# Kernel optimization log

Hardware: AMD Instinct MI355X
Metric: run time of the kernel (lower is better)

## Reference

```python
import jax, jax.numpy as jnp
import numpy as np

N_NODES = 50000
N_EDGES = 800000
GNN_IN, GNN_HID, COMB = 256, 64, 64
MLP_IN, MLP_HID = 256, 512


def glorot(key, shape):
    fan_in, fan_out = shape[0], shape[1]
    s = jnp.sqrt(6.0 / (fan_in + fan_out)).astype(jnp.float32)
    return jax.random.uniform(key, shape, jnp.float32, -s, s)


def setup_inputs() -> dict:
    key = jax.random.key(0)
    ks = jax.random.split(key, 12)
    x = jax.random.normal(ks[0], (N_NODES, GNN_IN), jnp.float32)
    edge_index = jax.random.randint(ks[1], (2, N_EDGES), 0, N_NODES, jnp.int64 if jax.config.jax_enable_x64 else jnp.int32)
    edge_attr = jax.random.uniform(ks[2], (N_EDGES,), jnp.float32)
    user_features = jax.random.normal(ks[3], (N_NODES, MLP_IN), jnp.float32)
    params = {
        'gcn1_W': glorot(ks[4], (GNN_IN, GNN_HID)),
        'gcn1_b': jnp.zeros((GNN_HID,), jnp.float32),
        'gcn2_W': glorot(ks[5], (GNN_HID, COMB)),
        'gcn2_b': jnp.zeros((COMB,), jnp.float32),
        'fc1_W': glorot(ks[6], (MLP_IN, MLP_HID)),
        'fc1_b': jnp.zeros((MLP_HID,), jnp.float32),
        'fc2_W': glorot(ks[7], (MLP_HID, COMB)),
        'fc2_b': jnp.zeros((COMB,), jnp.float32),
        'fcf_W': glorot(ks[8], (2 * COMB, 1)),
        'fcf_b': jnp.zeros((1,), jnp.float32),
    }
    return dict(x=x, edge_index=edge_index, edge_attr=edge_attr,
                user_features=user_features, **params)


def gcn_conv(x, W, b, src, dst, ew, n_nodes):
    # PyG GCNConv: transform, add self-loops (weight 1), sym-normalize, scatter-add.
    h = x @ W  # [N, out]
    loop = jnp.arange(n_nodes, dtype=src.dtype)
    src_sl = jnp.concatenate([src, loop])
    dst_sl = jnp.concatenate([dst, loop])
    ew_sl = jnp.concatenate([ew, jnp.ones((n_nodes,), ew.dtype)])
    deg = jax.ops.segment_sum(ew_sl, dst_sl, num_segments=n_nodes)
    dinv = jnp.where(deg > 0, jax.lax.rsqrt(jnp.maximum(deg, 1e-12)), 0.0)
    norm = dinv[src_sl] * ew_sl * dinv[dst_sl]  # [E+N]
    msg = h[src_sl] * norm[:, None]             # gather + scale
    out = jax.ops.segment_sum(msg, dst_sl, num_segments=n_nodes)
    return out + b


def reference(x, edge_index, edge_attr, user_features,
              gcn1_W, gcn1_b, gcn2_W, gcn2_b,
              fc1_W, fc1_b, fc2_W, fc2_b, fcf_W, fcf_b):
    src, dst = edge_index[0], edge_index[1]
    n = x.shape[0]
    # MLP branch
    mlp_out = jax.nn.relu(user_features @ fc1_W + fc1_b) @ fc2_W + fc2_b
    # GNN branch
    g = gcn_conv(x, gcn1_W, gcn1_b, src, dst, edge_attr, n)
    g = jax.nn.relu(g)
    gnn_out = gcn_conv(g, gcn2_W, gcn2_b, src, dst, edge_attr, n)
    combined = jnp.concatenate([mlp_out, gnn_out], axis=-1)
    return combined @ fcf_W + fcf_b
```

## Files before the change

kernel.cpp:

```cpp
#include <hip/hip_runtime.h>
#include <hip/hip_bf16.h>

#define N_NODES 50000
#define N_EDGES 800000
#define BROW 264
#define NT_TILES 782
#define GRID_MLP 256
#define GRID_H13 512

typedef __attribute__((ext_vector_type(8))) short bfrag8;
typedef __attribute__((ext_vector_type(4))) float f32x4;
typedef __attribute__((ext_vector_type(4))) unsigned short us4;
typedef __attribute__((ext_vector_type(8))) unsigned short us8;

__device__ __forceinline__ float bf2f(unsigned short u) {
  return __uint_as_float(((unsigned int)u) << 16);
}
__device__ __forceinline__ unsigned short f2bf(float f) {
  unsigned int u = __float_as_uint(f);
  u = (u + 0x7fffu + ((u >> 16) & 1u)) >> 16;
  return (unsigned short)u;
}
__device__ __forceinline__ float ldS(const void* p, int f32, size_t i) {
  return f32 ? ((const float*)p)[i] : bf2f(((const unsigned short*)p)[i]);
}
__device__ __forceinline__ void stO(void* out, int f32, int i, float v) {
  if (f32) ((float*)out)[i] = v;
  else ((unsigned short*)out)[i] = f2bf(v);
}

__device__ __forceinline__ void stageLoadBF(const void* src, int nb, us8 st[4]) {
  const int t = threadIdx.x;
  const int r = t & 63, q = t >> 6;
  int row = nb + r; row = row < N_NODES ? row : (N_NODES - 1);
  const us8* s8 = (const us8*)((const unsigned short*)src + (size_t)row * 256 + q * 32);
#pragma unroll
  for (int j = 0; j < 4; ++j) st[j] = s8[j];
}
__device__ __forceinline__ void stageWrite(const us8 st[4], unsigned short* __restrict__ Bs) {
  const int t = threadIdx.x;
  const int r = t & 63, q = t >> 6;
  unsigned short* dst = Bs + r * BROW + q * 32;
#pragma unroll
  for (int j = 0; j < 4; ++j) *(us8*)(dst + j * 8) = st[j];
}
__device__ __forceinline__ void stageF32(const void* src, int nb,
                                         unsigned short* __restrict__ Bs) {
  const int t = threadIdx.x;
  const int r = t & 63, q = t >> 6;
  int row = nb + r; row = row < N_NODES ? row : (N_NODES - 1);
  const f32x4* s4 = (const f32x4*)((const float*)src + (size_t)row * 256 + q * 32);
  unsigned short* dst = Bs + r * BROW + q * 32;
#pragma unroll
  for (int j = 0; j < 4; ++j) {
    f32x4 a = s4[2 * j], b = s4[2 * j + 1];
    us8 o;
    o[0] = f2bf(a[0]); o[1] = f2bf(a[1]); o[2] = f2bf(a[2]); o[3] = f2bf(a[3]);
    o[4] = f2bf(b[0]); o[5] = f2bf(b[1]); o[6] = f2bf(b[2]); o[7] = f2bf(b[3]);
    *(us8*)(dst + j * 8) = o;
  }
}

__global__ void k_detect(const void* x, const void* ea, const void* uf,
                         const void* f1W, const int* ei, int* flags) {
  int lane = threadIdx.x & 63;
  unsigned short ux = ((const unsigned short*)x)[lane];
  unsigned short ue = ((const unsigned short*)ea)[lane];
  unsigned short uu = ((const unsigned short*)uf)[lane];
  unsigned short uw = ((const unsigned short*)f1W)[lane];
  int oi = ei[2 * lane + 1];
  unsigned long long bx = __ballot(((ux >> 7) & 0xFF) > 0x85);
  unsigned long long be = __ballot((ue & 0x8000u) != 0);
  unsigned long long bu = __ballot(((uu >> 7) & 0xFF) > 0x85);
  unsigned long long bw = __ballot(((uw >> 7) & 0xFF) > 0x7E);
  unsigned long long bi = __ballot(oi != 0);
  if (lane == 0) {
    int fx = bx ? 1 : 0, fe = be ? 1 : 0, fu = bu ? 1 : 0, fw = bw ? 1 : 0;
    flags[0] = fx; flags[1] = fe; flags[2] = fu; flags[3] = fw;
    flags[4] = (bi == 0ull) ? 1 : 0;
    flags[5] = (fx & fe & fu & fw);
  }
}

__global__ __launch_bounds__(256) void k_zeroc(int* __restrict__ counts) {
  int i = blockIdx.x * 256 + threadIdx.x;
  if (i <= N_NODES) counts[i] = 0;
}

__global__ __launch_bounds__(256) void k_histpos(const int* __restrict__ ei,
                                                 const int* __restrict__ flags,
                                                 int* __restrict__ counts,
                                                 int* __restrict__ posw) {
  int e = blockIdx.x * 256 + threadIdx.x;
  if (e >= N_EDGES) return;
  int d;
  if (flags[4]) d = ei[1600000 + 2 * e];
  else          d = ei[800000 + e];
  d = d < 0 ? 0 : (d > N_NODES - 1 ? N_NODES - 1 : d);
  posw[e] = atomicAdd(&counts[d], 1);
}

__global__ __launch_bounds__(256) void k_scan1(const int* __restrict__ cnt,
                                               int* __restrict__ rp,
                                               int* __restrict__ bsum) {
  __shared__ int sd[256];
  int t = threadIdx.x;
  int i0 = blockIdx.x * 1024 + t * 4;
  int v0 = (i0 + 0) < N_NODES ? cnt[i0 + 0] : 0;
  int v1 = (i0 + 1) < N_NODES ? cnt[i0 + 1] : 0;
  int v2 = (i0 + 2) < N_NODES ? cnt[i0 + 2] : 0;
  int v3 = (i0 + 3) < N_NODES ? cnt[i0 + 3] : 0;
  int ts = v0 + v1 + v2 + v3;
  sd[t] = ts;
  __syncthreads();
  for (int off = 1; off < 256; off <<= 1) {
    int x = (t >= off) ? sd[t - off] : 0;
    __syncthreads();
    sd[t] += x;
    __syncthreads();
  }
  int exoff = sd[t] - ts;
  if (i0 + 0 < N_NODES) rp[i0 + 0] = exoff;
  if (i0 + 1 < N_NODES) rp[i0 + 1] = exoff + v0;
  if (i0 + 2 < N_NODES) rp[i0 + 2] = exoff + v0 + v1;
  if (i0 + 3 < N_NODES) rp[i0 + 3] = exoff + v0 + v1 + v2;
  if (t == 255) bsum[blockIdx.x] = sd[255];
}

__global__ void k_scan2(const int* __restrict__ bsum, int* __restrict__ boff,
                        int* __restrict__ rp, int nb) {
  if (threadIdx.x == 0) {
    int run = 0;
    for (int b = 0; b < nb; ++b) { boff[b] = run; run += bsum[b]; }
    rp[N_NODES] = run;
  }
}

__global__ __launch_bounds__(256) void k_scan3(int* __restrict__ rp,
                                               const int* __restrict__ boff) {
  int i = blockIdx.x * 256 + threadIdx.x;
  if (i < N_NODES) rp[i] += boff[i >> 10];
}

__global__ __launch_bounds__(256) void k_placeb(const int* __restrict__ ei,
                                                const void* ea,
                                                const int* __restrict__ flags,
                                                const int* __restrict__ rp,
                                                const int* __restrict__ posw,
                                                unsigned long long* __restrict__ e8) {
  int e = blockIdx.x * 256 + threadIdx.x;
  if (e >= N_EDGES) return;
  int s, d;
  if (flags[4]) { s = ei[2 * e]; d = ei[1600000 + 2 * e]; }
  else          { s = ei[e];     d = ei[800000 + e]; }
  s = s < 0 ? 0 : (s > N_NODES - 1 ? N_NODES - 1 : s);
  d = d < 0 ? 0 : (d > N_NODES - 1 ? N_NODES - 1 : d);
  float w = ldS(ea, flags[1], e);
  int pos = rp[d] + posw[e];
  e8[pos] = ((unsigned long long)__float_as_uint(w) << 32) | (unsigned int)s;
}

__global__ __launch_bounds__(256) void k_degc(const int* __restrict__ rp,
                                              const unsigned long long* __restrict__ e8,
                                              float* __restrict__ dinv) {
  const int i = blockIdx.x * 4 + (threadIdx.x >> 6);
  if (i >= N_NODES) return;
  const int lane = threadIdx.x & 63;
  const int base = rp[i], end = rp[i + 1];
  float s = 0.f;
  for (int j = base + lane; j < end; j += 64)
    s += __uint_as_float((unsigned int)(e8[j] >> 32));
#pragma unroll
  for (int off = 32; off > 0; off >>= 1) s += __shfl_xor(s, off, 64);
  if (lane == 0) dinv[i] = rsqrtf(s + 1.0f);
}

__global__ __launch_bounds__(512) void k_prep(
    const void* f1W, const void* g1W, const void* f2W, const void* f2b,
    const void* g2W, const void* g2b, const void* ffW, const void* ffb,
    const int* __restrict__ flags, unsigned short* __restrict__ W1T,
    unsigned short* __restrict__ WgT, float* __restrict__ w2f,
    float* __restrict__ w2g, float* __restrict__ constv) {
  const int fw = flags[3];
  if (blockIdx.x < 288) {
    int tid = blockIdx.x * 512 + threadIdx.x;
    if (tid < 512 * 256) {
      int c = tid >> 8, k = tid & 255;
      W1T[tid] = f2bf(ldS(f1W, fw, (size_t)k * 512 + c));
    } else if (tid < 512 * 256 + 64 * 256) {
      int j = tid - 512 * 256;
      int c = j >> 8, k = j & 255;
      WgT[j] = f2bf(ldS(g1W, fw, (size_t)k * 64 + c));
    }
    return;
  }
  int t = threadIdx.x;
  if (t < 512) {
    float s = 0.f;
    for (int c = 0; c < 64; ++c) s += ldS(f2W, fw, t * 64 + c) * ldS(ffW, fw, c);
    w2f[t] = s;
  }
  if (t < 64) {
    float s = 0.f;
    for (int c = 0; c < 64; ++c) s += ldS(g2W, fw, t * 64 + c) * ldS(ffW, fw, 64 + c);
    w2g[t] = s;
  }
  if (t == 0) {
    float s = ldS(ffb, fw, 0);
    for (int c = 0; c < 64; ++c) {
      s += ldS(f2b, fw, c) * ldS(ffW, fw, c);
      s += ldS(g2b, fw, c) * ldS(ffW, fw, 64 + c);
    }
    constv[0] = s;
  }
}

__global__ __launch_bounds__(512, 2) void k_h13P(
    const void* x, const unsigned short* __restrict__ WgT,
    const float* __restrict__ dinv, const int* __restrict__ flags,
    unsigned short* __restrict__ h1b) {
  __shared__ __align__(16) unsigned short Bs[2][64 * BROW];
  const int f32in = flags[0];
  const int lane = threadIdx.x & 63;
  const int wave = threadIdx.x >> 6;
  const int ct = wave & 3;
  const int nh = wave >> 2;
  const int l15 = lane & 15;
  const int quad = lane >> 4;

  bfrag8 A[8];
  {
    const unsigned short* ap = WgT + (size_t)(ct * 16 + l15) * 256 + quad * 8;
#pragma unroll
    for (int ks = 0; ks < 8; ++ks) A[ks] = *(const bfrag8*)(ap + ks * 32);
  }

  int tile = blockIdx.x;
  if (f32in) stageF32(x, tile * 64, Bs[0]);
  else { us8 st[4]; stageLoadBF(x, tile * 64, st); stageWrite(st, Bs[0]); }
  __syncthreads();

  int cur = 0;
  for (; tile < NT_TILES; tile += GRID_H13) {
    const int nxt = tile + GRID_H13;
    const bool have = nxt < NT_TILES;
    us8 st[4];
    if (!f32in && have) stageLoadBF(x, nxt * 64, st);

    f32x4 acc[2];
    acc[0] = (f32x4){0.f, 0.f, 0.f, 0.f};
    acc[1] = (f32x4){0.f, 0.f, 0.f, 0.f};
    const unsigned short* Bc = Bs[cur];
#pragma unroll
    for (int ks = 0; ks < 8; ++ks) {
      const int bofs = ks * 32 + quad * 8;
#pragma unroll
      for (int u = 0; u < 2; ++u) {
        bfrag8 b = *(const bfrag8*)(Bc + (nh * 32 + u * 16 + l15) * BROW + bofs);
        acc[u] = __builtin_amdgcn_mfma_f32_16x16x32_bf16(A[ks], b, acc[u], 0, 0, 0);
      }
    }

    if (have) {
      if (f32in) stageF32(x, nxt * 64, Bs[cur ^ 1]);
      else       stageWrite(st, Bs[cur ^ 1]);
    }

#pragma unroll
    for (int u = 0; u < 2; ++u) {
      int node = tile * 64 + nh * 32 + u * 16 + l15;
      if (node < N_NODES) {
        float di = dinv[node];
        us4 o;
#pragma unroll
        for (int r = 0; r < 4; ++r) o[r] = f2bf(acc[u][r] * di);
        *(us4*)(h1b + (size_t)node * 64 + ct * 16 + quad * 4) = o;
      }
    }
    __syncthreads();
    cur ^= 1;
  }
}

__global__ __launch_bounds__(512, 2) void k_mlpP(
    const void* uf, const unsigned short* __restrict__ W1T,
    const void* fc1b, const float* __restrict__ w2f,
    const int* __restrict__ flags, float* __restrict__ mlpc) {
  __shared__ __align__(16) unsigned short Bs[2][64 * BROW];
  __shared__ float red[2][512];
  const int f32in = flags[2];
  const int fw = flags[3];
  const int lane = threadIdx.x & 63;
  const int wave = threadIdx.x >> 6;
  const int l15 = lane & 15;
  const int quad = lane >> 4;
  const int c_base = wave * 64;

  bfrag8 A[4][8];
  {
    const unsigned short* ap = W1T + (size_t)(c_base + l15) * 256 + quad * 8;
#pragma unroll
    for (int t = 0; t < 4; ++t)
#pragma unroll
      for (int ks = 0; ks < 8; ++ks)
        A[t][ks] = *(const bfrag8*)(ap + (size_t)t * 16 * 256 + ks * 32);
  }

  int tile = blockIdx.x;
  if (f32in) stageF32(uf, tile * 64, Bs[0]);
  else { us8 st[4]; stageLoadBF(uf, tile * 64, st); stageWrite(st, Bs[0]); }
  __syncthreads();

  int cur = 0, pp = 0;
  for (; tile < NT_TILES; tile += GRID_MLP) {
    const int nxt = tile + GRID_MLP;
    const bool have = nxt < NT_TILES;
    us8 st[4];
    if (!f32in && have) stageLoadBF(uf, nxt * 64, st);

    f32x4 acc[4][4];
#pragma unroll
    for (int t = 0; t < 4; ++t)
#pragma unroll
      for (int u = 0; u < 4; ++u) acc[t][u] = (f32x4){0.f, 0.f, 0.f, 0.f};

    const unsigned short* Bc = Bs[cur];
#pragma unroll
    for (int ks = 0; ks < 8; ++ks) {
      const int bofs = ks * 32 + quad * 8;
      bfrag8 b[4];
#pragma unroll
      for (int u = 0; u < 4; ++u)
        b[u] = *(const bfrag8*)(Bc + (u * 16 + l15) * BROW + bofs);
#pragma unroll
      for (int t = 0; t < 4; ++t)
#pragma unroll
        for (int u = 0; u < 4; ++u)
          acc[t][u] = __builtin_amdgcn_mfma_f32_16x16x32_bf16(A[t][ks], b[u], acc[t][u], 0, 0, 0);
    }

    float part[4] = {0.f, 0.f, 0.f, 0.f};
#pragma unroll
    for (int t = 0; t < 4; ++t) {
#pragma unroll
      for (int r = 0; r < 4; ++r) {
        const int c = c_base + t * 16 + quad * 4 + r;
        const float bc = ldS(fc1b, fw, c);
        const float wc = w2f[c];
#pragma unroll
        for (int u = 0; u < 4; ++u) {
          float v = acc[t][u][r] + bc;
          v = v > 0.f ? v : 0.f;
          part[u] += v * wc;
        }
      }
    }

    if (have) {
      if (f32in) stageF32(uf, nxt * 64, Bs[cur ^ 1]);
      else       stageWrite(st, Bs[cur ^ 1]);
    }

#pragma unroll
    for (int u = 0; u < 4; ++u) {
      part[u] += __shfl_xor(part[u], 16, 64);
      part[u] += __shfl_xor(part[u], 32, 64);
      if (lane < 16) red[pp][wave * 64 + u * 16 + l15] = part[u];
    }
    __syncthreads();
    if (threadIdx.x < 64) {
      float sum = 0.f;
#pragma unroll
      for (int w = 0; w < 8; ++w) sum += red[pp][w * 64 + threadIdx.x];
      int node = tile * 64 + threadIdx.x;
      if (node < N_NODES) mlpc[node] = sum;
    }
    cur ^= 1; pp ^= 1;
  }
}

__global__ __launch_bounds__(256) void k_aggs2(
    const int* __restrict__ rp, const unsigned long long* __restrict__ e8,
    const unsigned short* __restrict__ h1b, const float* __restrict__ dinv,
    const void* g1b, const float* __restrict__ w2g,
    const int* __restrict__ flags, float* __restrict__ s2) {
  const int i = blockIdx.x * 4 + (threadIdx.x >> 6);
  if (i >= N_NODES) return;
  const int lane = threadIdx.x & 63;
  const int base = rp[i], end = rp[i + 1];
  const float di = dinv[i];
  float acc = 0.f;
  int j = base;
  for (; j + 8 <= end; j += 8) {
    unsigned long long vv[8];
#pragma unroll
    for (int q = 0; q < 8; ++q) vv[q] = e8[j + q];
    float ww[8], hv[8];
#pragma unroll
    for (int q = 0; q < 8; ++q) {
      ww[q] = __uint_as_float((unsigned int)(vv[q] >> 32));
      hv[q] = bf2f(h1b[(size_t)(unsigned int)vv[q] * 64 + lane]);
    }
#pragma unroll
    for (int q = 0; q < 8; ++q) acc += ww[q] * hv[q];
  }
  for (; j < end; ++j) {
    unsigned long long v = e8[j];
    acc += __uint_as_float((unsigned int)(v >> 32)) *
           bf2f(h1b[(size_t)(unsigned int)v * 64 + lane]);
  }
  float v = (acc + bf2f(h1b[(size_t)i * 64 + lane])) * di + ldS(g1b, flags[3], lane);
  v = v > 0.f ? v : 0.f;
  float p = v * w2g[lane];
#pragma unroll
  for (int off = 32; off > 0; off >>= 1) p += __shfl_xor(p, off, 64);
  if (lane == 0) s2[i] = di * p;
}

__global__ __launch_bounds__(256) void k_fin2(
    const int* __restrict__ rp, const unsigned long long* __restrict__ e8,
    const float* __restrict__ s2, const float* __restrict__ dinv,
    const float* __restrict__ mlpc, const float* __restrict__ constv,
    const int* __restrict__ flags, void* out) {
  const int i = blockIdx.x * 4 + (threadIdx.x >> 6);
  if (i >= N_NODES) return;
  const int lane = threadIdx.x & 63;
  const int base = rp[i], end = rp[i + 1];
  float p = 0.f;
  for (int j = base + lane; j < end; j += 64) {
    unsigned long long v = e8[j];
    p += __uint_as_float((unsigned int)(v >> 32)) * s2[(unsigned int)v];
  }
#pragma unroll
  for (int off = 32; off > 0; off >>= 1) p += __shfl_xor(p, off, 64);
  if (lane == 0) {
    float di = dinv[i];
    stO(out, flags[5], i, mlpc[i] + di * (p + s2[i]) + constv[0]);
  }
}

__global__ __launch_bounds__(256) void k_zero(const int* __restrict__ flags, void* out) {
  int i = blockIdx.x * 256 + threadIdx.x;
  if (i < N_NODES) stO(out, flags[5], i, 0.f);
}

extern "C" void kernel_launch(void* const* d_in, const int* in_sizes, int n_in,
                              void* d_out, int out_size, void* d_ws, size_t ws_size,
                              hipStream_t stream) {
  const void* x   = d_in[0];
  const int*  ei  = (const int*)d_in[1];
  const void* ea  = d_in[2];
  const void* uf  = d_in[3];
  const void* g1W = d_in[4];
  const void* g1b = d_in[5];
  const void* g2W = d_in[6];
  const void* g2b = d_in[7];
  const void* f1W = d_in[8];
  const void* f1b = d_in[9];
  const void* f2W = d_in[10];
  const void* f2b = d_in[11];
  const void* ffW = d_in[12];
  const void* ffb = d_in[13];

  float* ws = (float*)d_ws;
  int*   flags  = (int*)ws;
  float* w2f    = ws + 16;
  float* w2g    = ws + 528;
  float* constv = ws + 592;
  float* dinv   = ws + 608;
  float* s2     = ws + 50608;
  float* mlpc   = ws + 100608;
  unsigned short* W1T = (unsigned short*)(ws + 150608);
  unsigned short* WgT = W1T + 131072;
  int* rowptr = (int*)(ws + 224336);
  int* bsum   = (int*)(ws + 274352);
  int* boff   = bsum + 64;
  int* counts = (int*)(ws + 274480);
  int* posw   = (int*)(ws + 324496);
  unsigned long long* e8 = (unsigned long long*)(ws + 1124496);
  unsigned short* h1b = (unsigned short*)(ws + 2724496);
  const size_t NEED = (size_t)4324496 * 4;

  k_detect<<<1, 64, 0, stream>>>(x, ea, uf, f1W, ei, flags);
  if (ws_size < NEED) {
    k_zero<<<(N_NODES + 255) / 256, 256, 0, stream>>>(flags, d_out);
    return;
  }
  const int NZB = (N_NODES + 256) / 256;
  const int NB  = (N_NODES + 1023) / 1024;
  const int NEB = (N_EDGES + 255) / 256;

  k_zeroc<<<NZB, 256, 0, stream>>>(counts);
  k_histpos<<<NEB, 256, 0, stream>>>(ei, flags, counts, posw);
  k_scan1<<<NB, 256, 0, stream>>>(counts, rowptr, bsum);
  k_scan2<<<1, 64, 0, stream>>>(bsum, boff, rowptr, NB);
  k_scan3<<<(N_NODES + 255) / 256, 256, 0, stream>>>(rowptr, boff);
  k_placeb<<<NEB, 256, 0, stream>>>(ei, ea, flags, rowptr, posw, e8);
  k_degc<<<(N_NODES + 3) / 4, 256, 0, stream>>>(rowptr, e8, dinv);
  k_prep<<<289, 512, 0, stream>>>(f1W, g1W, f2W, f2b, g2W, g2b, ffW, ffb, flags,
                                  W1T, WgT, w2f, w2g, constv);
  k_h13P<<<GRID_H13, 512, 0, stream>>>(x, WgT, dinv, flags, h1b);
  k_mlpP<<<GRID_MLP, 512, 0, stream>>>(uf, W1T, f1b, w2f, flags, mlpc);
  k_aggs2<<<(N_NODES + 3) / 4, 256, 0, stream>>>(rowptr, e8, h1b, dinv, g1b, w2g, flags, s2);
  k_fin2<<<(N_NODES + 3) / 4, 256, 0, stream>>>(rowptr, e8, s2, dinv, mlpc, constv, flags, d_out);
}
```

Measured before the change: 352.3 us.

## Split MLP hidden dimension across two block halves with separate partial outputs

The MLP kernel now launches 1024 blocks, and each half handles 256 of the 512 hidden columns. Every wave keeps 32 columns of W1 in registers instead of 64, and the two partial dot products go to separate buffers that the final kernel adds together. The goal is more parallelism and lower register pressure, which should raise occupancy on a GPU with many CUs. The cost is that each user-feature tile is now loaded twice, and the prefetch of the next tile no longer overlaps with the MFMA work.

After: 359.1 us. About the same (+1.9%).

```diff
diff --git a/kernel.cpp b/kernel.cpp
--- a/kernel.cpp
+++ b/kernel.cpp
@@ -5,7 +5,6 @@
 #define N_EDGES 800000
 #define BROW 264
 #define NT_TILES 782
-#define GRID_MLP 256
 #define GRID_H13 512
 
 typedef __attribute__((ext_vector_type(8))) short bfrag8;
@@ -282,45 +281,46 @@
   }
 }
 
-__global__ __launch_bounds__(512, 2) void k_mlpP(
+__global__ __launch_bounds__(512, 2) void k_mlpH(
     const void* uf, const unsigned short* __restrict__ W1T,
     const void* fc1b, const float* __restrict__ w2f,
-    const int* __restrict__ flags, float* __restrict__ mlpc) {
+    const int* __restrict__ flags, float* __restrict__ mlpc,
+    float* __restrict__ mlpc2) {
   __shared__ __align__(16) unsigned short Bs[2][64 * BROW];
   __shared__ float red[2][512];
   const int f32in = flags[2];
   const int fw = flags[3];
+  const int half = blockIdx.x >> 9;
+  const int bid = blockIdx.x & 511;
   const int lane = threadIdx.x & 63;
   const int wave = threadIdx.x >> 6;
   const int l15 = lane & 15;
   const int quad = lane >> 4;
-  const int c_base = wave * 64;
-
-  bfrag8 A[4][8];
+  const int c_base = half * 256 + wave * 32;
+  float* __restrict__ mout = half ? mlpc2 : mlpc;
+
+  bfrag8 A[2][8];
   {
     const unsigned short* ap = W1T + (size_t)(c_base + l15) * 256 + quad * 8;
 #pragma unroll
-    for (int t = 0; t < 4; ++t)
+    for (int t = 0; t < 2; ++t)
 #pragma unroll
       for (int ks = 0; ks < 8; ++ks)
         A[t][ks] = *(const bfrag8*)(ap + (size_t)t * 16 * 256 + ks * 32);
   }
 
-  int tile = blockIdx.x;
-  if (f32in) stageF32(uf, tile * 64, Bs[0]);
-  else { us8 st[4]; stageLoadBF(uf, tile * 64, st); stageWrite(st, Bs[0]); }
+  if (f32in) stageF32(uf, bid * 64, Bs[0]);
+  else { us8 st[4]; stageLoadBF(uf, bid * 64, st); stageWrite(st, Bs[0]); }
   __syncthreads();
 
   int cur = 0, pp = 0;
-  for (; tile < NT_TILES; tile += GRID_MLP) {
-    const int nxt = tile + GRID_MLP;
+  for (int tile = bid; tile < NT_TILES; tile += 512) {
+    const int nxt = tile + 512;
     const bool have = nxt < NT_TILES;
-    us8 st[4];
-    if (!f32in && have) stageLoadBF(uf, nxt * 64, st);
-
-    f32x4 acc[4][4];
-#pragma unroll
-    for (int t = 0; t < 4; ++t)
+
+    f32x4 acc[2][4];
+#pragma unroll
+    for (int t = 0; t < 2; ++t)
 #pragma unroll
       for (int u = 0; u < 4; ++u) acc[t][u] = (f32x4){0.f, 0.f, 0.f, 0.f};
 
@@ -333,7 +333,7 @@
       for (int u = 0; u < 4; ++u)
         b[u] = *(const bfrag8*)(Bc + (u * 16 + l15) * BROW + bofs);
 #pragma unroll
-      for (int t = 0; t < 4; ++t)
+      for (int t = 0; t < 2; ++t)
 #pragma unroll
         for (int u = 0; u < 4; ++u)
           acc[t][u] = __builtin_amdgcn_mfma_f32_16x16x32_bf16(A[t][ks], b[u], acc[t][u], 0, 0, 0);
@@ -341,7 +341,7 @@
 
     float part[4] = {0.f, 0.f, 0.f, 0.f};
 #pragma unroll
-    for (int t = 0; t < 4; ++t) {
+    for (int t = 0; t < 2; ++t)
 #pragma unroll
       for (int r = 0; r < 4; ++r) {
         const int c = c_base + t * 16 + quad * 4 + r;
@@ -354,11 +354,10 @@
           part[u] += v * wc;
         }
       }
-    }
 
     if (have) {
       if (f32in) stageF32(uf, nxt * 64, Bs[cur ^ 1]);
-      else       stageWrite(st, Bs[cur ^ 1]);
+      else { us8 st[4]; stageLoadBF(uf, nxt * 64, st); stageWrite(st, Bs[cur ^ 1]); }
     }
 
 #pragma unroll
@@ -373,7 +372,7 @@
 #pragma unroll
       for (int w = 0; w < 8; ++w) sum += red[pp][w * 64 + threadIdx.x];
       int node = tile * 64 + threadIdx.x;
-      if (node < N_NODES) mlpc[node] = sum;
+      if (node < N_NODES) mout[node] = sum;
     }
     cur ^= 1; pp ^= 1;
   }
@@ -420,8 +419,8 @@
 __global__ __launch_bounds__(256) void k_fin2(
     const int* __restrict__ rp, const unsigned long long* __restrict__ e8,
     const float* __restrict__ s2, const float* __restrict__ dinv,
-    const float* __restrict__ mlpc, const float* __restrict__ constv,
-    const int* __restrict__ flags, void* out) {
+    const float* __restrict__ mlpc, const float* __restrict__ mlpc2,
+    const float* __restrict__ constv, const int* __restrict__ flags, void* out) {
   const int i = blockIdx.x * 4 + (threadIdx.x >> 6);
   if (i >= N_NODES) return;
   const int lane = threadIdx.x & 63;
@@ -435,7 +434,7 @@
   for (int off = 32; off > 0; off >>= 1) p += __shfl_xor(p, off, 64);
   if (lane == 0) {
     float di = dinv[i];
-    stO(out, flags[5], i, mlpc[i] + di * (p + s2[i]) + constv[0]);
+    stO(out, flags[5], i, mlpc[i] + mlpc2[i] + di * (p + s2[i]) + constv[0]);
   }
 }
 
@@ -479,7 +478,8 @@
   int* posw   = (int*)(ws + 324496);
   unsigned long long* e8 = (unsigned long long*)(ws + 1124496);
   unsigned short* h1b = (unsigned short*)(ws + 2724496);
-  const size_t NEED = (size_t)4324496 * 4;
+  float* mlpc2 = ws + 4324496;
+  const size_t NEED = (size_t)4374496 * 4;
 
   k_detect<<<1, 64, 0, stream>>>(x, ea, uf, f1W, ei, flags);
   if (ws_size < NEED) {
@@ -500,7 +500,7 @@
   k_prep<<<289, 512, 0, stream>>>(f1W, g1W, f2W, f2b, g2W, g2b, ffW, ffb, flags,
                                   W1T, WgT, w2f, w2g, constv);
   k_h13P<<<GRID_H13, 512, 0, stream>>>(x, WgT, dinv, flags, h1b);
-  k_mlpP<<<GRID_MLP, 512, 0, stream>>>(uf, W1T, f1b, w2f, flags, mlpc);
+  k_mlpH<<<1024, 512, 0, stream>>>(uf, W1T, f1b, w2f, flags, mlpc, mlpc2);
   k_aggs2<<<(N_NODES + 3) / 4, 256, 0, stream>>>(rowptr, e8, h1b, dinv, g1b, w2g, flags, s2);
-  k_fin2<<<(N_NODES + 3) / 4, 256, 0, stream>>>(rowptr, e8, s2, dinv, mlpc, constv, flags, d_out);
-}
+  k_fin2<<<(N_NODES + 3) / 4, 256, 0, stream>>>(rowptr, e8, s2, dinv, mlpc, mlpc2, constv, flags, d_out);
+}
```
